# Kernel tuning notes

Hardware: AMD Instinct MI355X
Metric: run time of the kernel (lower is better)

Reference implementation:

```python
import jax, jax.numpy as jnp
import numpy as np

N = 50000      # nodes
E = 800000     # edges (before self-loops)
IN = 256       # in_channels
OUT = 64       # out_channels
H = 4          # heads (conv1)
NC = 10        # num_classes
NEG = 0.2      # LeakyReLU negative slope (PyG default)


def setup_inputs() -> dict:
    key = jax.random.key(0)
    ks = jax.random.split(key, 12)

    def w(k, shape, fan_in):
        return jax.random.normal(k, shape, jnp.float32) / np.sqrt(fan_in).astype(np.float32)

    x = jax.random.normal(ks[0], (N, IN), jnp.float32)
    edge_index = jax.random.randint(ks[1], (2, E), 0, N)
    return dict(
        x=x, edge_index=edge_index,
        Wl1=w(ks[2], (IN, H * OUT), IN), Wr1=w(ks[3], (IN, H * OUT), IN),
        att1=w(ks[4], (H, OUT), OUT), b1=jnp.zeros((H * OUT,), jnp.float32),
        Wl2=w(ks[5], (H * OUT, OUT), H * OUT), Wr2=w(ks[6], (H * OUT, OUT), H * OUT),
        att2=w(ks[7], (1, OUT), OUT), b2=jnp.zeros((OUT,), jnp.float32),
        Wlin=w(ks[8], (OUT, NC), OUT), blin=jnp.zeros((NC,), jnp.float32),
    )


def _gatv2(x, src, dst, Wl, Wr, att, bias, heads, out_ch, concat):
    """GATv2Conv (eval mode): gather, LeakyReLU score, segment-softmax over dst, scatter-add."""
    n = x.shape[0]
    xl = (x @ Wl).reshape(n, heads, out_ch)   # source-side transform [N,H,C]
    xr = (x @ Wr).reshape(n, heads, out_ch)   # target-side transform [N,H,C]
    e = jax.nn.leaky_relu(xl[src] + xr[dst], NEG)          # [E',H,C]
    score = jnp.einsum('ehc,hc->eh', e, att)               # [E',H]
    m = jax.ops.segment_max(score, dst, num_segments=n)    # stable softmax per target node
    a = jnp.exp(score - m[dst])
    s = jax.ops.segment_sum(a, dst, num_segments=n)
    alpha = a / s[dst]                                     # [E',H]
    out = jax.ops.segment_sum(alpha[:, :, None] * xl[src], dst, num_segments=n)  # [N,H,C]
    out = out.reshape(n, heads * out_ch) if concat else out.mean(axis=1)
    return out + bias


def reference(x, edge_index, Wl1, Wr1, att1, b1, Wl2, Wr2, att2, b2, Wlin, blin):
    n = x.shape[0]
    loop = jnp.arange(n, dtype=edge_index.dtype)           # PyG add_self_loops=True
    src = jnp.concatenate([edge_index[0], loop])
    dst = jnp.concatenate([edge_index[1], loop])
    h = jax.nn.relu(_gatv2(x, src, dst, Wl1, Wr1, att1, b1, H, OUT, True))
    h = jax.nn.relu(_gatv2(h, src, dst, Wl2, Wr2, att2, b2, 1, OUT, False))
    return h @ Wlin + blin
```

## Files before the change

### kernel.cpp

```cpp
#include <hip/hip_runtime.h>
#include <hip/hip_fp16.h>
#include <math.h>

#define NEG_SLOPE 0.2f

typedef _Float16 f16x8 __attribute__((ext_vector_type(8)));
typedef float f32x4  __attribute__((ext_vector_type(4)));
typedef float f32x2  __attribute__((ext_vector_type(2)));
typedef _Float16 h2v __attribute__((ext_vector_type(2)));

union U8 { uint4 u; f16x8 v; h2v h[4]; };

#if defined(__has_builtin)
#if __has_builtin(__builtin_amdgcn_global_load_lds)
#define HAS_GLL 1
#endif
#endif
#ifndef HAS_GLL
#define HAS_GLL 0
#endif

#if HAS_GLL
typedef __attribute__((address_space(1))) const unsigned int GU;
typedef __attribute__((address_space(3))) unsigned int LU;
#endif

__device__ __forceinline__ f16x8 lrelu8(f16x8 s){
    return __builtin_elementwise_max(s, s * (_Float16)NEG_SLOPE);
}
__device__ __forceinline__ float fdot2f(h2v a, h2v b, float c){
#if __has_builtin(__builtin_amdgcn_fdot2)
    return __builtin_amdgcn_fdot2(a, b, c, false);
#else
    return c + (float)a[0]*(float)b[0] + (float)a[1]*(float)b[1];
#endif
}

__global__ void cvtinit_k(int Nn,
                          int* __restrict__ cnt, int* __restrict__ items,
                          const float* __restrict__ Wl1, const float* __restrict__ Wr1,
                          const float* __restrict__ Wl2, const float* __restrict__ Wr2,
                          const float* __restrict__ att1, const float* __restrict__ att2,
                          const float* __restrict__ Wlin,
                          _Float16* __restrict__ bt1, _Float16* __restrict__ bt2,
                          _Float16* __restrict__ a1h, _Float16* __restrict__ a2h,
                          _Float16* __restrict__ WtH)
{
    int t = blockIdx.x*256 + threadIdx.x;
    if (t < Nn){
        cnt[t] = 1;
        items[t << 6] = t;
        return;
    }
    int u = t - Nn;
    if (u < 512*256){
        int k = u & 255, nn = u >> 8;
        float v = (nn < 256) ? Wl1[(size_t)k*256 + nn] : Wr1[(size_t)k*256 + (nn-256)];
        bt1[u] = (_Float16)v;
        return;
    }
    u -= 512*256;
    if (u < 128*256){
        int k = u & 255, nn = u >> 8;
        float v = (nn < 64) ? Wl2[(size_t)k*64 + nn] : Wr2[(size_t)k*64 + (nn-64)];
        bt2[u] = (_Float16)v;
        return;
    }
    u -= 128*256;
    if (u < 256){ a1h[u] = (_Float16)att1[u]; return; }
    u -= 256;
    if (u < 64){ a2h[u] = (_Float16)att2[u]; return; }
    u -= 64;
    if (u < 640){
        int c = u >> 6, ch = u & 63;
        WtH[u] = (_Float16)Wlin[ch*10 + c];
    }
}

__global__ __launch_bounds__(256) void prep_k(
    const float* __restrict__ Af, const _Float16* __restrict__ Bt,
    _Float16* __restrict__ C, int M, int GB,
    const int* __restrict__ src, const int* __restrict__ dst, int E,
    int* __restrict__ cnt, int* __restrict__ items)
{
    __shared__ __align__(16) _Float16 sA[64*256];
    __shared__ __align__(16) _Float16 sB[128*32];

    int t = threadIdx.x;
    if ((int)blockIdx.x >= GB){
        int e = ((int)blockIdx.x - GB)*256 + t;
        if (e < E){
            int d = dst[e];
            int pos = atomicAdd(&cnt[d], 1);
            items[(d << 6) + pos] = src[e];
        }
        return;
    }

    int lane = t & 63, wave = t >> 6;
    int wm = (wave >> 1) * 32, wn = (wave & 1) * 64;
    int lm = lane & 15, kq = lane >> 4;
    int m0 = blockIdx.x * 64;

    #pragma unroll
    for (int it = 0; it < 8; ++it){
        int g = it*256 + t;
        int r = g >> 5, c = g & 31;
        U8 hv; hv.u = make_uint4(0u,0u,0u,0u);
        if (m0 + r < M){
            const float* gp = Af + (size_t)(m0 + r)*256 + c*8;
            float4 f0 = *reinterpret_cast<const float4*>(gp);
            float4 f1 = *reinterpret_cast<const float4*>(gp + 4);
            hv.v[0]=(_Float16)f0.x; hv.v[1]=(_Float16)f0.y;
            hv.v[2]=(_Float16)f0.z; hv.v[3]=(_Float16)f0.w;
            hv.v[4]=(_Float16)f1.x; hv.v[5]=(_Float16)f1.y;
            hv.v[6]=(_Float16)f1.z; hv.v[7]=(_Float16)f1.w;
        }
        *reinterpret_cast<uint4*>(sA + r*256 + ((c ^ (r & 31)) << 3)) = hv.u;
    }

    int r0 = t >> 2, s0 = (t & 3) * 8;

    for (int n0 = 0; n0 < 512; n0 += 128){
        f32x4 acc[2][4] = {};
        for (int kc = 0; kc < 256; kc += 32){
            __syncthreads();
#if HAS_GLL
            {
                const _Float16* gB0 = Bt + (size_t)(n0 + r0)*256 + kc + s0;
                const _Float16* gB1 = Bt + (size_t)(n0 + r0 + 64)*256 + kc + s0;
                __builtin_amdgcn_global_load_lds((GU*)gB0, (LU*)(sB + t*8), 16, 0, 0);
                __builtin_amdgcn_global_load_lds((GU*)gB1, (LU*)(sB + (t+256)*8), 16, 0, 0);
            }
#else
            #pragma unroll
            for (int it = 0; it < 2; ++it){
                int idx = t + 256*it;
                int rr = idx >> 2, ss = (idx & 3) * 8;
                *reinterpret_cast<uint4*>(sB + rr*32 + ss) =
                    *reinterpret_cast<const uint4*>(Bt + (size_t)(n0 + rr)*256 + kc + ss);
            }
#endif
            __syncthreads();

            f16x8 fa[2], fb[4];
            #pragma unroll
            for (int i = 0; i < 2; ++i){
                int row = wm + i*16 + lm;
                int ck  = (kc >> 3) + kq;
                fa[i] = *reinterpret_cast<const f16x8*>(sA + row*256 + ((ck ^ (row & 31)) << 3));
            }
            #pragma unroll
            for (int j = 0; j < 4; ++j)
                fb[j] = *reinterpret_cast<const f16x8*>(sB + (wn + j*16 + lm)*32 + kq*8);
            #pragma unroll
            for (int i = 0; i < 2; ++i)
                #pragma unroll
                for (int j = 0; j < 4; ++j)
                    acc[i][j] = __builtin_amdgcn_mfma_f32_16x16x32_f16(fa[i], fb[j], acc[i][j], 0, 0, 0);
        }

        #pragma unroll
        for (int i = 0; i < 2; ++i){
            #pragma unroll
            for (int r = 0; r < 4; ++r){
                int m = m0 + wm + i*16 + kq*4 + r;
                if (m < M){
                    #pragma unroll
                    for (int j = 0; j < 4; ++j)
                        C[(size_t)m*512 + n0 + wn + j*16 + lm] = (_Float16)acc[i][j][r];
                }
            }
        }
    }
}

__global__ __launch_bounds__(256) void gemm2_k(
    const _Float16* __restrict__ A, const _Float16* __restrict__ Bt,
    _Float16* __restrict__ C, int M, int Ntot, int K)
{
    __shared__ __align__(16) _Float16 sA[128*32];
    __shared__ __align__(16) _Float16 sB[128*32];

    int t = threadIdx.x;
    int lane = t & 63, wave = t >> 6;
    int wm = (wave >> 1) * 64, wn = (wave & 1) * 64;
    int m0 = blockIdx.y * 128, n0 = blockIdx.x * 128;
    int lm = lane & 15, kq = lane >> 4;

    int r0 = t >> 2, s0 = (t & 3) * 8;

    f32x4 acc[4][4] = {};

    for (int kc = 0; kc < K; kc += 32){
        __syncthreads();
#if HAS_GLL
        {
            const _Float16* gA0 = A + (size_t)(m0 + r0)*K + kc + s0;
            const _Float16* gA1 = A + (size_t)(m0 + r0 + 64)*K + kc + s0;
            const _Float16* gB0 = Bt + (size_t)(n0 + r0)*K + kc + s0;
            const _Float16* gB1 = Bt + (size_t)(n0 + r0 + 64)*K + kc + s0;
            if (m0 + r0 < M)
                __builtin_amdgcn_global_load_lds((GU*)gA0, (LU*)(sA + t*8), 16, 0, 0);
            if (m0 + r0 + 64 < M)
                __builtin_amdgcn_global_load_lds((GU*)gA1, (LU*)(sA + (t+256)*8), 16, 0, 0);
            __builtin_amdgcn_global_load_lds((GU*)gB0, (LU*)(sB + t*8), 16, 0, 0);
            __builtin_amdgcn_global_load_lds((GU*)gB1, (LU*)(sB + (t+256)*8), 16, 0, 0);
        }
#else
        #pragma unroll
        for (int it = 0; it < 2; ++it){
            int idx = t + 256*it;
            int rr = idx >> 2, ss = (idx & 3) * 8;
            uint4 va = make_uint4(0u,0u,0u,0u);
            if (m0 + rr < M)
                va = *reinterpret_cast<const uint4*>(A + (size_t)(m0 + rr)*K + kc + ss);
            *reinterpret_cast<uint4*>(sA + rr*32 + ss) = va;
            *reinterpret_cast<uint4*>(sB + rr*32 + ss) =
                *reinterpret_cast<const uint4*>(Bt + (size_t)(n0 + rr)*K + kc + ss);
        }
#endif
        __syncthreads();

        f16x8 fa[4], fb[4];
        #pragma unroll
        for (int i = 0; i < 4; ++i){
            fa[i] = *reinterpret_cast<const f16x8*>(sA + (wm + i*16 + lm)*32 + kq*8);
            fb[i] = *reinterpret_cast<const f16x8*>(sB + (wn + i*16 + lm)*32 + kq*8);
        }
        #pragma unroll
        for (int i = 0; i < 4; ++i)
            #pragma unroll
            for (int j = 0; j < 4; ++j)
                acc[i][j] = __builtin_amdgcn_mfma_f32_16x16x32_f16(fa[i], fb[j], acc[i][j], 0, 0, 0);
    }

    #pragma unroll
    for (int i = 0; i < 4; ++i){
        #pragma unroll
        for (int r = 0; r < 4; ++r){
            int m = m0 + wm + i*16 + kq*4 + r;
            if (m < M){
                #pragma unroll
                for (int j = 0; j < 4; ++j)
                    C[(size_t)m*Ntot + n0 + wn + j*16 + lm] = (_Float16)acc[i][j][r];
            }
        }
    }
}

__global__ __launch_bounds__(256) void agg1_k(
    const _Float16* __restrict__ xlr,
    const int* __restrict__ cnt, const int* __restrict__ items,
    const _Float16* __restrict__ attH, const float* __restrict__ bias,
    _Float16* __restrict__ h1, int Nn)
{
    int wave = threadIdx.x >> 6, lane = threadIdx.x & 63;
    int i = blockIdx.x*4 + wave;
    if (i >= Nn) return;
    int q = lane >> 4, r = lane & 15;

    const uint4* x4 = reinterpret_cast<const uint4*>(xlr);
    uint ib = (uint)i * 64u;
    U8 xra, xrb, ata, atb;
    xra.u = x4[ib + 32u + (uint)r*2u];
    xrb.u = x4[ib + 32u + (uint)r*2u + 1u];
    const uint4* a4 = reinterpret_cast<const uint4*>(attH);
    ata.u = a4[r*2]; atb.u = a4[r*2+1];

    int beg = i << 6;
    int n   = cnt[i];

    f32x2 acc2[8];
    #pragma unroll
    for (int k = 0; k < 8; ++k) acc2[k] = (f32x2){0.f, 0.f};
    float l = 0.f;

    auto idxld = [&](int j)->uint {
        int jj = (j < n) ? j : (n-1);
        return (uint)items[beg + jj] * 64u;
    };

    uint sA = idxld(q), sB = idxld(q+4);
    U8 a0, a1, b0, b1;
    a0.u = x4[sA + (uint)r*2u]; a1.u = x4[sA + (uint)r*2u + 1u];
    b0.u = x4[sB + (uint)r*2u]; b1.u = x4[sB + (uint)r*2u + 1u];

    for (int j = 0; j < n; j += 8){
        uint sA2 = idxld(j+8+q), sB2 = idxld(j+12+q);
        U8 p0, p1, p2, p3;
        p0.u = x4[sA2 + (uint)r*2u]; p1.u = x4[sA2 + (uint)r*2u + 1u];
        p2.u = x4[sB2 + (uint)r*2u]; p3.u = x4[sB2 + (uint)r*2u + 1u];

        U8 tA0, tA1, tB0, tB1;
        tA0.v = lrelu8(a0.v + xra.v);
        tA1.v = lrelu8(a1.v + xrb.v);
        tB0.v = lrelu8(b0.v + xra.v);
        tB1.v = lrelu8(b1.v + xrb.v);
        float pA = 0.f, pB = 0.f;
        #pragma unroll
        for (int k = 0; k < 4; ++k){
            pA = fdot2f(tA0.h[k], ata.h[k], pA);
            pB = fdot2f(tB0.h[k], ata.h[k], pB);
        }
        #pragma unroll
        for (int k = 0; k < 4; ++k){
            pA = fdot2f(tA1.h[k], atb.h[k], pA);
            pB = fdot2f(tB1.h[k], atb.h[k], pB);
        }
        pA += __shfl_xor(pA, 1, 64);  pB += __shfl_xor(pB, 1, 64);
        pA += __shfl_xor(pA, 2, 64);  pB += __shfl_xor(pB, 2, 64);
        float wA = (j+q   < n) ? __expf(pA) : 0.f;
        float wB = (j+4+q < n) ? __expf(pB) : 0.f;
        l += wA + wB;
        f32x2 wA2 = {wA, wA}, wB2 = {wB, wB};
        #pragma unroll
        for (int k = 0; k < 4; ++k){
            acc2[k]   += wA2 * __builtin_convertvector(a0.h[k], f32x2)
                       + wB2 * __builtin_convertvector(b0.h[k], f32x2);
            acc2[k+4] += wA2 * __builtin_convertvector(a1.h[k], f32x2)
                       + wB2 * __builtin_convertvector(b1.h[k], f32x2);
        }
        a0 = p0; a1 = p1; b0 = p2; b1 = p3;
    }

    #pragma unroll
    for (int k = 0; k < 8; ++k){
        acc2[k][0] += __shfl_xor(acc2[k][0], 16, 64);
        acc2[k][1] += __shfl_xor(acc2[k][1], 16, 64);
        acc2[k][0] += __shfl_xor(acc2[k][0], 32, 64);
        acc2[k][1] += __shfl_xor(acc2[k][1], 32, 64);
    }
    l += __shfl_xor(l, 16, 64);
    l += __shfl_xor(l, 32, 64);

    if (q == 0){
        float inv = 1.f / l;
        U8 o0, o1;
        #pragma unroll
        for (int k = 0; k < 8; ++k){
            o0.v[k] = (_Float16)fmaxf(acc2[k>>1][k&1]*inv + bias[r*16 + k], 0.f);
            o1.v[k] = (_Float16)fmaxf(acc2[4+(k>>1)][k&1]*inv + bias[r*16 + 8 + k], 0.f);
        }
        uint4* h4 = reinterpret_cast<uint4*>(h1);
        h4[(uint)i*32u + (uint)r*2u]      = o0.u;
        h4[(uint)i*32u + (uint)r*2u + 1u] = o1.u;
    }
}

__global__ __launch_bounds__(256) void agg2_k(
    const _Float16* __restrict__ xlr,
    const int* __restrict__ cnt, const int* __restrict__ items,
    const _Float16* __restrict__ attH, const float* __restrict__ bias,
    const _Float16* __restrict__ WtH, const float* __restrict__ blin,
    float* __restrict__ out, int Nn)
{
    int wave = threadIdx.x >> 6, lane = threadIdx.x & 63;
    int g = lane >> 3, r = lane & 7;
    int i0 = blockIdx.x*32 + wave*8 + g;
    bool ok = (i0 < Nn);
    int i = ok ? i0 : (Nn-1);

    const uint4* x4 = reinterpret_cast<const uint4*>(xlr);
    U8 xr, at;
    xr.u = x4[(uint)i*16u + 8u + (uint)r];
    at.u = reinterpret_cast<const uint4*>(attH)[r];

    int beg = i << 6;
    int n   = cnt[i];

    auto idxOf = [&](int j)->uint {
        int jj = (j < n) ? j : (n-1);
        return (uint)items[beg + jj] * 16u;
    };

    float acc[8];
    #pragma unroll
    for (int k = 0; k < 8; ++k) acc[k] = 0.f;
    float l = 0.f;

    uint iA0 = idxOf(0), iB0 = idxOf(1);
    U8 vA, vB;
    vA.u = x4[iA0 + (uint)r];
    vB.u = x4[iB0 + (uint)r];
    uint iA1 = idxOf(2), iB1 = idxOf(3);

    for (int j = 0; j < n; j += 2){
        uint iA2 = idxOf(j+4), iB2 = idxOf(j+5);
        U8 pA, pB;
        pA.u = x4[iA1 + (uint)r];
        pB.u = x4[iB1 + (uint)r];

        U8 tA; tA.v = lrelu8(vA.v + xr.v);
        U8 tB; tB.v = lrelu8(vB.v + xr.v);
        float p1 = 0.f, p2 = 0.f;
        #pragma unroll
        for (int k = 0; k < 4; ++k){
            p1 = fdot2f(tA.h[k], at.h[k], p1);
            p2 = fdot2f(tB.h[k], at.h[k], p2);
        }
        p1 += __shfl_xor(p1, 1, 64);  p2 += __shfl_xor(p2, 1, 64);
        p1 += __shfl_xor(p1, 2, 64);  p2 += __shfl_xor(p2, 2, 64);
        p1 += __shfl_xor(p1, 4, 64);  p2 += __shfl_xor(p2, 4, 64);
        float wA = __expf(p1);
        float wB = (j+1 < n) ? __expf(p2) : 0.f;
        l += wA + wB;
        #pragma unroll
        for (int k = 0; k < 8; ++k)
            acc[k] += wA * (float)vA.v[k] + wB * (float)vB.v[k];
        vA = pA; vB = pB; iA1 = iA2; iB1 = iB2;
    }

    float inv = 1.f / l;
    U8 o;
    #pragma unroll
    for (int k = 0; k < 8; ++k)
        o.v[k] = (_Float16)fmaxf(acc[k]*inv + bias[r*8 + k], 0.f);

    const uint4* w4 = reinterpret_cast<const uint4*>(WtH);
    #pragma unroll
    for (int c = 0; c < 10; ++c){
        U8 wv; wv.u = w4[c*8 + r];
        float p = 0.f;
        #pragma unroll
        for (int k = 0; k < 4; ++k) p = fdot2f(o.h[k], wv.h[k], p);
        p += __shfl_xor(p, 1, 64);
        p += __shfl_xor(p, 2, 64);
        p += __shfl_xor(p, 4, 64);
        if (ok && r == (c & 7))
            out[(size_t)i0*10 + c] = p + blin[c];
    }
}


extern "C" void kernel_launch(void* const* d_in, const int* in_sizes, int n_in,
                              void* d_out, int out_size, void* d_ws, size_t ws_size,
                              hipStream_t stream)
{
    const float* x    = (const float*)d_in[0];
    const int*   ei   = (const int*)  d_in[1];
    const float* Wl1  = (const float*)d_in[2];
    const float* Wr1  = (const float*)d_in[3];
    const float* att1 = (const float*)d_in[4];
    const float* b1   = (const float*)d_in[5];
    const float* Wl2  = (const float*)d_in[6];
    const float* Wr2  = (const float*)d_in[7];
    const float* att2 = (const float*)d_in[8];
    const float* b2   = (const float*)d_in[9];
    const float* Wlin = (const float*)d_in[10];
    const float* blin = (const float*)d_in[11];
    float* out = (float*)d_out;

    const int N = in_sizes[0] / 256;
    const int E = in_sizes[1] / 2;
    const int K = 256;
    const int* srcp = ei;
    const int* dstp = ei + E;

    char* ws = (char*)d_ws;
    size_t off = 0;
    auto alloc = [&](size_t bytes)->char*{
        char* p = ws + off;
        off += (bytes + 255) & ~(size_t)255;
        return p;
    };
    _Float16* xlr1 = (_Float16*)alloc((size_t)N*512*2);
    _Float16* xlr2 = (_Float16*)alloc((size_t)N*128*2);
    _Float16* h1   = (_Float16*)alloc((size_t)N*256*2);
    _Float16* bt1  = (_Float16*)alloc((size_t)512*K*2);
    _Float16* bt2  = (_Float16*)alloc((size_t)128*K*2);
    _Float16* a1h  = (_Float16*)alloc(256*2);
    _Float16* a2h  = (_Float16*)alloc(64*2);
    _Float16* WtH  = (_Float16*)alloc(640*2);
    int* cnt   = (int*)alloc((size_t)N*4);
    int* items = (int*)alloc((size_t)N*64*4);
    (void)ws_size;

    const int eb = (E + 255) / 256;
    const int gb = (N + 63) / 64;

    const int cvt_total = N + 512*256 + 128*256 + 256 + 64 + 640;
    hipLaunchKernelGGL(cvtinit_k, dim3((cvt_total + 255)/256), dim3(256), 0, stream,
                       N, cnt, items, Wl1, Wr1, Wl2, Wr2, att1, att2, Wlin,
                       bt1, bt2, a1h, a2h, WtH);

    hipLaunchKernelGGL(prep_k, dim3(gb + eb), dim3(256), 0, stream,
                       x, bt1, xlr1, N, gb, srcp, dstp, E, cnt, items);

    hipLaunchKernelGGL(agg1_k, dim3((N+3)/4), dim3(256), 0, stream,
                       xlr1, cnt, items, a1h, b1, h1, N);

    hipLaunchKernelGGL(gemm2_k, dim3(1, (N+127)/128), dim3(256), 0, stream,
                       h1, bt2, xlr2, N, 128, K);
    hipLaunchKernelGGL(agg2_k, dim3((N+31)/32), dim3(256), 0, stream,
                       xlr2, cnt, items, a2h, b2, WtH, blin, out, N);
}
```

Measured before the change: 256.5 us.

## Fill adjacency slots with valid indices and parallelize agg2 across edges per wave

New measurement: 276.4 us. 1.08x slower.

```diff
diff --git a/kernel.cpp b/kernel.cpp
--- a/kernel.cpp
+++ b/kernel.cpp
@@ -10,6 +10,7 @@
 typedef _Float16 h2v __attribute__((ext_vector_type(2)));
 
 union U8 { uint4 u; f16x8 v; h2v h[4]; };
+union U4 { uint2 u; h2v h[2]; _Float16 v[4]; };
 
 #if defined(__has_builtin)
 #if __has_builtin(__builtin_amdgcn_global_load_lds)
@@ -26,6 +27,9 @@
 #endif
 
 __device__ __forceinline__ f16x8 lrelu8(f16x8 s){
+    return __builtin_elementwise_max(s, s * (_Float16)NEG_SLOPE);
+}
+__device__ __forceinline__ h2v lrelu2(h2v s){
     return __builtin_elementwise_max(s, s * (_Float16)NEG_SLOPE);
 }
 __device__ __forceinline__ float fdot2f(h2v a, h2v b, float c){
@@ -47,12 +51,16 @@
                           _Float16* __restrict__ WtH)
 {
     int t = blockIdx.x*256 + threadIdx.x;
-    if (t < Nn){
-        cnt[t] = 1;
-        items[t << 6] = t;
+    if (t <= Nn){
+        int idx = (t < Nn) ? t : 0;
+        int4 w = make_int4(idx, idx, idx, idx);
+        int4* p = reinterpret_cast<int4*>(items + ((size_t)t << 6));
+        #pragma unroll
+        for (int k = 0; k < 16; ++k) p[k] = w;
+        if (t < Nn) cnt[t] = 1;
         return;
     }
-    int u = t - Nn;
+    int u = t - (Nn + 1);
     if (u < 512*256){
         int k = u & 255, nn = u >> 8;
         float v = (nn < 256) ? Wl1[(size_t)k*256 + nn] : Wr1[(size_t)k*256 + (nn-256)];
@@ -276,18 +284,15 @@
     for (int k = 0; k < 8; ++k) acc2[k] = (f32x2){0.f, 0.f};
     float l = 0.f;
 
-    auto idxld = [&](int j)->uint {
-        int jj = (j < n) ? j : (n-1);
-        return (uint)items[beg + jj] * 64u;
-    };
-
-    uint sA = idxld(q), sB = idxld(q+4);
+    uint sA = (uint)items[beg + q] * 64u;
+    uint sB = (uint)items[beg + 4 + q] * 64u;
     U8 a0, a1, b0, b1;
     a0.u = x4[sA + (uint)r*2u]; a1.u = x4[sA + (uint)r*2u + 1u];
     b0.u = x4[sB + (uint)r*2u]; b1.u = x4[sB + (uint)r*2u + 1u];
 
     for (int j = 0; j < n; j += 8){
-        uint sA2 = idxld(j+8+q), sB2 = idxld(j+12+q);
+        uint sA2 = (uint)items[beg + j + 8 + q] * 64u;
+        uint sB2 = (uint)items[beg + j + 12 + q] * 64u;
         U8 p0, p1, p2, p3;
         p0.u = x4[sA2 + (uint)r*2u]; p1.u = x4[sA2 + (uint)r*2u + 1u];
         p2.u = x4[sB2 + (uint)r*2u]; p3.u = x4[sB2 + (uint)r*2u + 1u];
@@ -322,6 +327,7 @@
                        + wB2 * __builtin_convertvector(b1.h[k], f32x2);
         }
         a0 = p0; a1 = p1; b0 = p2; b1 = p3;
+        sA = sA2; sB = sB2;
     }
 
     #pragma unroll
@@ -356,79 +362,92 @@
     float* __restrict__ out, int Nn)
 {
     int wave = threadIdx.x >> 6, lane = threadIdx.x & 63;
-    int g = lane >> 3, r = lane & 7;
-    int i0 = blockIdx.x*32 + wave*8 + g;
-    bool ok = (i0 < Nn);
-    int i = ok ? i0 : (Nn-1);
-
-    const uint4* x4 = reinterpret_cast<const uint4*>(xlr);
-    U8 xr, at;
-    xr.u = x4[(uint)i*16u + 8u + (uint)r];
-    at.u = reinterpret_cast<const uint4*>(attH)[r];
+    int i = blockIdx.x*4 + wave;
+    if (i >= Nn) return;
+    int q = lane >> 4, r = lane & 15;
+
+    const uint2* x2 = reinterpret_cast<const uint2*>(xlr);
+    U4 xr, at;
+    xr.u = x2[(uint)i*32u + 16u + (uint)r];
+    at.u = reinterpret_cast<const uint2*>(attH)[r];
 
     int beg = i << 6;
     int n   = cnt[i];
 
-    auto idxOf = [&](int j)->uint {
-        int jj = (j < n) ? j : (n-1);
-        return (uint)items[beg + jj] * 16u;
-    };
-
-    float acc[8];
-    #pragma unroll
-    for (int k = 0; k < 8; ++k) acc[k] = 0.f;
+    f32x2 acc2[2];
+    acc2[0] = (f32x2){0.f, 0.f};
+    acc2[1] = (f32x2){0.f, 0.f};
     float l = 0.f;
 
-    uint iA0 = idxOf(0), iB0 = idxOf(1);
-    U8 vA, vB;
-    vA.u = x4[iA0 + (uint)r];
-    vB.u = x4[iB0 + (uint)r];
-    uint iA1 = idxOf(2), iB1 = idxOf(3);
-
-    for (int j = 0; j < n; j += 2){
-        uint iA2 = idxOf(j+4), iB2 = idxOf(j+5);
-        U8 pA, pB;
-        pA.u = x4[iA1 + (uint)r];
-        pB.u = x4[iB1 + (uint)r];
-
-        U8 tA; tA.v = lrelu8(vA.v + xr.v);
-        U8 tB; tB.v = lrelu8(vB.v + xr.v);
-        float p1 = 0.f, p2 = 0.f;
-        #pragma unroll
-        for (int k = 0; k < 4; ++k){
-            p1 = fdot2f(tA.h[k], at.h[k], p1);
-            p2 = fdot2f(tB.h[k], at.h[k], p2);
-        }
-        p1 += __shfl_xor(p1, 1, 64);  p2 += __shfl_xor(p2, 1, 64);
-        p1 += __shfl_xor(p1, 2, 64);  p2 += __shfl_xor(p2, 2, 64);
-        p1 += __shfl_xor(p1, 4, 64);  p2 += __shfl_xor(p2, 4, 64);
-        float wA = __expf(p1);
-        float wB = (j+1 < n) ? __expf(p2) : 0.f;
+    uint sA = (uint)items[beg + q] * 32u;
+    uint sB = (uint)items[beg + 4 + q] * 32u;
+    U4 a0, b0;
+    a0.u = x2[sA + (uint)r];
+    b0.u = x2[sB + (uint)r];
+
+    for (int j = 0; j < n; j += 8){
+        uint sA2 = (uint)items[beg + j + 8 + q] * 32u;
+        uint sB2 = (uint)items[beg + j + 12 + q] * 32u;
+        U4 p0, p1;
+        p0.u = x2[sA2 + (uint)r];
+        p1.u = x2[sB2 + (uint)r];
+
+        U4 tA, tB;
+        tA.h[0] = lrelu2(a0.h[0] + xr.h[0]);
+        tA.h[1] = lrelu2(a0.h[1] + xr.h[1]);
+        tB.h[0] = lrelu2(b0.h[0] + xr.h[0]);
+        tB.h[1] = lrelu2(b0.h[1] + xr.h[1]);
+        float pA = fdot2f(tA.h[0], at.h[0], 0.f);
+        float pB = fdot2f(tB.h[0], at.h[0], 0.f);
+        pA = fdot2f(tA.h[1], at.h[1], pA);
+        pB = fdot2f(tB.h[1], at.h[1], pB);
+        pA += __shfl_xor(pA, 1, 64);  pB += __shfl_xor(pB, 1, 64);
+        pA += __shfl_xor(pA, 2, 64);  pB += __shfl_xor(pB, 2, 64);
+        pA += __shfl_xor(pA, 4, 64);  pB += __shfl_xor(pB, 4, 64);
+        pA += __shfl_xor(pA, 8, 64);  pB += __shfl_xor(pB, 8, 64);
+        float wA = (j+q   < n) ? __expf(pA) : 0.f;
+        float wB = (j+4+q < n) ? __expf(pB) : 0.f;
         l += wA + wB;
-        #pragma unroll
-        for (int k = 0; k < 8; ++k)
-            acc[k] += wA * (float)vA.v[k] + wB * (float)vB.v[k];
-        vA = pA; vB = pB; iA1 = iA2; iB1 = iB2;
-    }
+        f32x2 wA2 = {wA, wA}, wB2 = {wB, wB};
+        acc2[0] += wA2 * __builtin_convertvector(a0.h[0], f32x2)
+                 + wB2 * __builtin_convertvector(b0.h[0], f32x2);
+        acc2[1] += wA2 * __builtin_convertvector(a0.h[1], f32x2)
+                 + wB2 * __builtin_convertvector(b0.h[1], f32x2);
+        a0 = p0; b0 = p1;
+        sA = sA2; sB = sB2;
+    }
+
+    #pragma unroll
+    for (int k = 0; k < 2; ++k){
+        acc2[k][0] += __shfl_xor(acc2[k][0], 16, 64);
+        acc2[k][1] += __shfl_xor(acc2[k][1], 16, 64);
+        acc2[k][0] += __shfl_xor(acc2[k][0], 32, 64);
+        acc2[k][1] += __shfl_xor(acc2[k][1], 32, 64);
+    }
+    l += __shfl_xor(l, 16, 64);
+    l += __shfl_xor(l, 32, 64);
 
     float inv = 1.f / l;
-    U8 o;
-    #pragma unroll
-    for (int k = 0; k < 8; ++k)
-        o.v[k] = (_Float16)fmaxf(acc[k]*inv + bias[r*8 + k], 0.f);
-
-    const uint4* w4 = reinterpret_cast<const uint4*>(WtH);
-    #pragma unroll
-    for (int c = 0; c < 10; ++c){
-        U8 wv; wv.u = w4[c*8 + r];
-        float p = 0.f;
-        #pragma unroll
-        for (int k = 0; k < 4; ++k) p = fdot2f(o.h[k], wv.h[k], p);
+    U4 o;
+    #pragma unroll
+    for (int k = 0; k < 4; ++k)
+        o.v[k] = (_Float16)fmaxf(acc2[k>>1][k&1]*inv + bias[r*4 + k], 0.f);
+
+    const uint2* w2 = reinterpret_cast<const uint2*>(WtH);
+    #pragma unroll
+    for (int s = 0; s < 3; ++s){
+        int c = q + s*4;
+        bool cok = (c < 10);
+        int cc = cok ? c : 0;
+        U4 wv; wv.u = w2[cc*16 + r];
+        float p = fdot2f(o.h[0], wv.h[0], 0.f);
+        p = fdot2f(o.h[1], wv.h[1], p);
         p += __shfl_xor(p, 1, 64);
         p += __shfl_xor(p, 2, 64);
         p += __shfl_xor(p, 4, 64);
-        if (ok && r == (c & 7))
-            out[(size_t)i0*10 + c] = p + blin[c];
+        p += __shfl_xor(p, 8, 64);
+        if (cok && r == 0)
+            out[(size_t)i*10 + c] = p + blin[c];
     }
 }
 
@@ -473,13 +492,13 @@
     _Float16* a2h  = (_Float16*)alloc(64*2);
     _Float16* WtH  = (_Float16*)alloc(640*2);
     int* cnt   = (int*)alloc((size_t)N*4);
-    int* items = (int*)alloc((size_t)N*64*4);
+    int* items = (int*)alloc(((size_t)N*64 + 64)*4);
     (void)ws_size;
 
     const int eb = (E + 255) / 256;
     const int gb = (N + 63) / 64;
 
-    const int cvt_total = N + 512*256 + 128*256 + 256 + 64 + 640;
+    const int cvt_total = (N + 1) + 512*256 + 128*256 + 256 + 64 + 640;
     hipLaunchKernelGGL(cvtinit_k, dim3((cvt_total + 255)/256), dim3(256), 0, stream,
                        N, cnt, items, Wl1, Wr1, Wl2, Wr2, att1, att2, Wlin,
                        bt1, bt2, a1h, a2h, WtH);
@@ -492,6 +511,6 @@
 
     hipLaunchKernelGGL(gemm2_k, dim3(1, (N+127)/128), dim3(256), 0, stream,
                        h1, bt2, xlr2, N, 128, K);
-    hipLaunchKernelGGL(agg2_k, dim3((N+31)/32), dim3(256), 0, stream,
+    hipLaunchKernelGGL(agg2_k, dim3((N+3)/4), dim3(256), 0, stream,
                        xlr2, cnt, items, a2h, b2, WtH, blin, out, N);
 }
```
